# Optimization experiments

Hardware: AMD Instinct MI355X
Metric: run time of the kernel (lower is better)

Reference implementation:

```python
import jax, jax.numpy as jnp
import numpy as np

B, S, D, H = 16, 2048, 128, 4
HD = D // H  # 32
EPS = 1e-5


def layer_norm(x, g, b):
    m = jnp.mean(x, axis=-1, keepdims=True)
    v = jnp.mean((x - m) ** 2, axis=-1, keepdims=True)
    return (x - m) * jax.lax.rsqrt(v + EPS) * g + b


def setup_inputs() -> dict:
    key = jax.random.key(0)
    ks = jax.random.split(key, 9)
    lin = lambda k: jax.random.normal(k, (D, D), dtype=jnp.float32) * 0.01  # [in, out]
    return {
        "input0": jax.random.normal(ks[0], (B, S, D), dtype=jnp.float32),
        "Wq": lin(ks[1]), "bq": jnp.zeros((D,), jnp.float32),
        "Wk": lin(ks[2]), "bk": jnp.zeros((D,), jnp.float32),
        "Wv": lin(ks[3]), "bv": jnp.zeros((D,), jnp.float32),
        "Wo": lin(ks[4]), "bo": jnp.zeros((D,), jnp.float32),
        "g1": jnp.ones((D,), jnp.float32), "b1": jnp.zeros((D,), jnp.float32),
        "W1": lin(ks[5]), "bf1": jnp.zeros((D,), jnp.float32),
        "W2": lin(ks[6]), "bf2": jnp.zeros((D,), jnp.float32),
        "g2": jnp.ones((D,), jnp.float32), "b2": jnp.zeros((D,), jnp.float32),
    }


def reference(input0, Wq, bq, Wk, bk, Wv, bv, Wo, bo, g1, b1, W1, bf1, W2, bf2, g2, b2):
    x = input0
    # multi-head attention (self-attention), dropout in eval mode (identity)
    q = (x @ Wq + bq).reshape(B, S, H, HD)
    k = (x @ Wk + bk).reshape(B, S, H, HD)
    v = (x @ Wv + bv).reshape(B, S, H, HD)
    scores = jnp.einsum("bqhd,bkhd->bhqk", q, k) / jnp.sqrt(jnp.float32(HD))
    weights = jax.nn.softmax(scores, axis=-1)
    attn = jnp.einsum("bhqk,bkhd->bqhd", weights, v).reshape(B, S, D)
    attn = attn @ Wo + bo
    attended = layer_norm(attn + x, g1, b1)
    # feed-forward; note residual uses x (not attended), faithful to source
    ff = jax.nn.relu(attended @ W1 + bf1) @ W2 + bf2
    return layer_norm(ff + x, g2, b2)
```

## Files before the change

kernel.cpp:

```cpp
#include <hip/hip_runtime.h>
#include <math.h>

#define NB   16
#define NS   2048
#define ND   128
#define NH   4
#define NHD  32
#define NROWS (NB * NS)

typedef unsigned short u16;
typedef __bf16 bf16x8 __attribute__((ext_vector_type(8)));
typedef float  f32x4  __attribute__((ext_vector_type(4)));
typedef float  f32x16 __attribute__((ext_vector_type(16)));

static __device__ __forceinline__ u16 f2bf(float a) {
    union { __bf16 h; u16 u; } t; t.h = (__bf16)a; return t.u;
}
static __device__ __forceinline__ unsigned int pk2(float a, float b) {
    union { __bf16 h[2]; unsigned int u; } t;
    t.h[0] = (__bf16)a; t.h[1] = (__bf16)b; return t.u;
}

#if __has_builtin(__builtin_amdgcn_exp2f)
#define EXP2(x) __builtin_amdgcn_exp2f(x)
#else
extern "C" __device__ float __ocml_native_exp2_f32(float);
#define EXP2(x) __ocml_native_exp2_f32(x)
#endif

#define QSCALE (0.17677669529663687f * 1.4426950408889634f)

__global__ __launch_bounds__(256) void prep_kernel(
    const float* __restrict__ x,
    const float* __restrict__ Wq, const float* __restrict__ Wk,
    const float* __restrict__ Wv, const float* __restrict__ Wo,
    const float* __restrict__ W1, const float* __restrict__ W2,
    u16* __restrict__ xb, u16* __restrict__ wt)
{
    const int blk = blockIdx.x, tid = threadIdx.x;
    if (blk < 2048) {
        size_t e0 = (size_t)blk * 2048 + (size_t)tid * 8;
        const float4* p = reinterpret_cast<const float4*>(x + e0);
        float4 f0 = p[0], f1 = p[1];
        int4 o;
        o.x = pk2(f0.x, f0.y); o.y = pk2(f0.z, f0.w);
        o.z = pk2(f1.x, f1.y); o.w = pk2(f1.z, f1.w);
        *reinterpret_cast<int4*>(xb + e0) = o;
    } else {
        const int wb   = blk - 2048;
        const int widx = wb >> 3, sub = wb & 7;
        const float* W = widx == 0 ? Wq : widx == 1 ? Wk : widx == 2 ? Wv
                       : widx == 3 ? Wo : widx == 4 ? W1 : W2;
        const int flat8 = sub * 256 + tid;
        const int n = flat8 >> 4, k0 = (flat8 & 15) * 8;
        float v[8];
        #pragma unroll
        for (int j = 0; j < 8; ++j) v[j] = W[(size_t)(k0 + j) * ND + n];
        int4 o;
        o.x = pk2(v[0], v[1]); o.y = pk2(v[2], v[3]);
        o.z = pk2(v[4], v[5]); o.w = pk2(v[6], v[7]);
        *reinterpret_cast<int4*>(wt + (size_t)widx * 16384 + (size_t)n * ND + k0) = o;
    }
}

__global__ __launch_bounds__(256) void qkv_mfma_kernel(
    const u16* __restrict__ xb,
    const u16* __restrict__ wtq, const u16* __restrict__ wtk, const u16* __restrict__ wtv,
    const float* __restrict__ bq, const float* __restrict__ bk, const float* __restrict__ bv,
    u16* __restrict__ qo, u16* __restrict__ kfo, u16* __restrict__ vfo)
{
    const int tid = threadIdx.x, lane = tid & 63, w = tid >> 6;
    const int n = lane & 15, c = lane >> 4;
    const int row0 = blockIdx.x * 64;
    const int grow = row0 + w * 16;

    bf16x8 a[4];
    #pragma unroll
    for (int kk = 0; kk < 4; ++kk)
        a[kk] = *reinterpret_cast<const bf16x8*>(xb + (size_t)(grow + n) * ND + kk * 32 + c * 8);

    f32x4 accq[8], acck[8], accv[8];
    #pragma unroll
    for (int nb = 0; nb < 8; ++nb) {
        accq[nb] = f32x4{0.f, 0.f, 0.f, 0.f};
        acck[nb] = f32x4{0.f, 0.f, 0.f, 0.f};
        accv[nb] = f32x4{0.f, 0.f, 0.f, 0.f};
    }

    #pragma unroll
    for (int kk = 0; kk < 4; ++kk) {
        #pragma unroll
        for (int nb = 0; nb < 8; ++nb) {
            const size_t boff = (size_t)(nb * 16 + n) * ND + kk * 32 + c * 8;
            bf16x8 bqf = *reinterpret_cast<const bf16x8*>(wtq + boff);
            bf16x8 bkf = *reinterpret_cast<const bf16x8*>(wtk + boff);
            bf16x8 bvf = *reinterpret_cast<const bf16x8*>(wtv + boff);
            accq[nb] = __builtin_amdgcn_mfma_f32_16x16x32_bf16(a[kk], bqf, accq[nb], 0, 0, 0);
            acck[nb] = __builtin_amdgcn_mfma_f32_16x16x32_bf16(a[kk], bkf, acck[nb], 0, 0, 0);
            accv[nb] = __builtin_amdgcn_mfma_f32_16x16x32_bf16(a[kk], bvf, accv[nb], 0, 0, 0);
        }
    }

    const int b   = row0 >> 11;
    const int sp0 = (row0 & (NS - 1)) + w * 16;

    #pragma unroll
    for (int nb = 0; nb < 8; ++nb) {
        const int col = nb * 16 + n, hh = col >> 5, d32 = col & 31;
        const float bqv = bq[col], bkv = bk[col], bvv = bv[col];
        const size_t kvb = ((size_t)b * NH + hh) * (NS * NHD);

        #pragma unroll
        for (int r = 0; r < 4; ++r)
            qo[kvb + (size_t)(sp0 + 4 * c + r) * NHD + d32] =
                f2bf((accq[nb][r] + bqv) * QSCALE);

        const int s = d32 >> 4, c2 = (d32 >> 3) & 1, j = d32 & 7;
        #pragma unroll
        for (int r = 0; r < 4; ++r) {
            const int key = sp0 + 4 * c + r;
            const int T = key >> 5, l5 = key & 31;
            kfo[kvb + (size_t)(T * 2 + s) * 512 + (size_t)(l5 + 32 * c2) * 8 + j] =
                f2bf(acck[nb][r] + bkv);
        }

        const int lanep = d32 + 32 * (c & 1);
        const int j0    = 4 * (c >> 1);
        float v0 = accv[nb][0] + bvv, v1 = accv[nb][1] + bvv;
        float v2 = accv[nb][2] + bvv, v3 = accv[nb][3] + bvv;
        *reinterpret_cast<uint2*>(
            vfo + kvb + (size_t)(sp0 >> 4) * 512 + (size_t)lanep * 8 + j0) =
            make_uint2(pk2(v0, v1), pk2(v2, v3));
    }
}

__global__ __launch_bounds__(256) void attn_mfma_kernel(
    const u16* __restrict__ qg,
    const u16* __restrict__ kfg,
    const u16* __restrict__ vfg,
    u16* __restrict__ ao)
{
    const int tid = threadIdx.x, lane = tid & 63, w = tid >> 6;
    const int bh = blockIdx.y, b = bh >> 2, h = bh & 3;
    const int n = lane & 31, hf = lane >> 5;
    const size_t fbase = (size_t)bh * (NS * NHD);
    const int q0w = blockIdx.x * 128 + w * 32;

    const bf16x8 qf0 = *reinterpret_cast<const bf16x8*>(
        qg + fbase + (size_t)(q0w + n) * NHD + 8 * hf);
    const bf16x8 qf1 = *reinterpret_cast<const bf16x8*>(
        qg + fbase + (size_t)(q0w + n) * NHD + 16 + 8 * hf);

    f32x16 ot, zz;
    #pragma unroll
    for (int i = 0; i < 16; ++i) { ot[i] = 0.f; zz[i] = 0.f; }
    float lp0 = 0.f, lp1 = 0.f, lp2 = 0.f, lp3 = 0.f;

    const u16* kf = kfg + fbase + (size_t)lane * 8;
    const u16* vf = vfg + fbase + (size_t)lane * 8;

    for (int t = 0; t < NS / 64; ++t) {
        const bf16x8 ka00 = *reinterpret_cast<const bf16x8*>(kf + (size_t)(4 * t + 0) * 512);
        const bf16x8 ka01 = *reinterpret_cast<const bf16x8*>(kf + (size_t)(4 * t + 1) * 512);
        const bf16x8 ka10 = *reinterpret_cast<const bf16x8*>(kf + (size_t)(4 * t + 2) * 512);
        const bf16x8 ka11 = *reinterpret_cast<const bf16x8*>(kf + (size_t)(4 * t + 3) * 512);
        const bf16x8 va0  = *reinterpret_cast<const bf16x8*>(vf + (size_t)(4 * t + 0) * 512);
        const bf16x8 va1  = *reinterpret_cast<const bf16x8*>(vf + (size_t)(4 * t + 1) * 512);
        const bf16x8 va2  = *reinterpret_cast<const bf16x8*>(vf + (size_t)(4 * t + 2) * 512);
        const bf16x8 va3  = *reinterpret_cast<const bf16x8*>(vf + (size_t)(4 * t + 3) * 512);

        f32x16 s0 = __builtin_amdgcn_mfma_f32_32x32x16_bf16(ka00, qf0, zz, 0, 0, 0);
        s0 = __builtin_amdgcn_mfma_f32_32x32x16_bf16(ka01, qf1, s0, 0, 0, 0);
        f32x16 s1 = __builtin_amdgcn_mfma_f32_32x32x16_bf16(ka10, qf0, zz, 0, 0, 0);
        s1 = __builtin_amdgcn_mfma_f32_32x32x16_bf16(ka11, qf1, s1, 0, 0, 0);

        {
            float p[16];
            #pragma unroll
            for (int r = 0; r < 16; ++r) p[r] = EXP2(s0[r]);
            lp0 += p[0] + p[4] + p[8]  + p[12];
            lp1 += p[1] + p[5] + p[9]  + p[13];
            lp2 += p[2] + p[6] + p[10] + p[14];
            lp3 += p[3] + p[7] + p[11] + p[15];
            union { unsigned int u[4]; bf16x8 v; } pw0, pw1;
            #pragma unroll
            for (int i = 0; i < 4; ++i) pw0.u[i] = pk2(p[2 * i], p[2 * i + 1]);
            #pragma unroll
            for (int i = 0; i < 4; ++i) pw1.u[i] = pk2(p[8 + 2 * i], p[9 + 2 * i]);
            ot = __builtin_amdgcn_mfma_f32_32x32x16_bf16(va0, pw0.v, ot, 0, 0, 0);
            ot = __builtin_amdgcn_mfma_f32_32x32x16_bf16(va1, pw1.v, ot, 0, 0, 0);
        }
        {
            float p[16];
            #pragma unroll
            for (int r = 0; r < 16; ++r) p[r] = EXP2(s1[r]);
            lp0 += p[0] + p[4] + p[8]  + p[12];
            lp1 += p[1] + p[5] + p[9]  + p[13];
            lp2 += p[2] + p[6] + p[10] + p[14];
            lp3 += p[3] + p[7] + p[11] + p[15];
            union { unsigned int u[4]; bf16x8 v; } pw0, pw1;
            #pragma unroll
            for (int i = 0; i < 4; ++i) pw0.u[i] = pk2(p[2 * i], p[2 * i + 1]);
            #pragma unroll
            for (int i = 0; i < 4; ++i) pw1.u[i] = pk2(p[8 + 2 * i], p[9 + 2 * i]);
            ot = __builtin_amdgcn_mfma_f32_32x32x16_bf16(va2, pw0.v, ot, 0, 0, 0);
            ot = __builtin_amdgcn_mfma_f32_32x32x16_bf16(va3, pw1.v, ot, 0, 0, 0);
        }
    }

    float lp = (lp0 + lp1) + (lp2 + lp3);
    const float dn  = lp + __shfl_xor(lp, 32);
    const float inv = 1.0f / dn;

    u16* orow = ao + ((size_t)b * NS + q0w + n) * ND + h * NHD + 4 * hf;
    #pragma unroll
    for (int g = 0; g < 4; ++g) {
        uint2 wv = make_uint2(pk2(ot[4 * g] * inv, ot[4 * g + 1] * inv),
                              pk2(ot[4 * g + 2] * inv, ot[4 * g + 3] * inv));
        *reinterpret_cast<uint2*>(orow + 8 * g) = wv;
    }
}

template <int MODE>
__global__ __launch_bounds__(256) void proj_kernel(
    const u16* __restrict__ A, const u16* __restrict__ Wt,
    const float* __restrict__ bias, const float* __restrict__ res,
    const float* __restrict__ gamma, const float* __restrict__ beta,
    u16* __restrict__ outb, float* __restrict__ outf)
{
    const int tid = threadIdx.x, lane = tid & 63, w = tid >> 6;
    const int n = lane & 15, c = lane >> 4;
    const int grow = blockIdx.x * 64 + w * 16;

    bf16x8 a[4];
    #pragma unroll
    for (int kk = 0; kk < 4; ++kk)
        a[kk] = *reinterpret_cast<const bf16x8*>(A + (size_t)(grow + n) * ND + kk * 32 + c * 8);

    f32x4 acc[8];
    #pragma unroll
    for (int nb = 0; nb < 8; ++nb) acc[nb] = f32x4{0.f, 0.f, 0.f, 0.f};

    #pragma unroll
    for (int kk = 0; kk < 4; ++kk) {
        #pragma unroll
        for (int nb = 0; nb < 8; ++nb) {
            bf16x8 bw = *reinterpret_cast<const bf16x8*>(
                Wt + (size_t)(nb * 16 + n) * ND + kk * 32 + c * 8);
            acc[nb] = __builtin_amdgcn_mfma_f32_16x16x32_bf16(a[kk], bw, acc[nb], 0, 0, 0);
        }
    }

    if (MODE == 2) {
        #pragma unroll
        for (int nb = 0; nb < 8; ++nb) {
            const int col = nb * 16 + n;
            const float bb = bias[col];
            #pragma unroll
            for (int r = 0; r < 4; ++r) {
                float vv = fmaxf(acc[nb][r] + bb, 0.f);
                outb[(size_t)(grow + 4 * c + r) * ND + col] = f2bf(vv);
            }
        }
    } else {
        float vals[8][4];
        float sr[4]  = {0.f, 0.f, 0.f, 0.f};
        float sr2[4] = {0.f, 0.f, 0.f, 0.f};
        #pragma unroll
        for (int nb = 0; nb < 8; ++nb) {
            const int col = nb * 16 + n;
            const float bb = bias[col];
            #pragma unroll
            for (int r = 0; r < 4; ++r) {
                float vv = acc[nb][r] + bb + res[(size_t)(grow + 4 * c + r) * ND + col];
                vals[nb][r] = vv;
                sr[r]  += vv;
                sr2[r] += vv * vv;
            }
        }
        #pragma unroll
        for (int m = 1; m < 16; m <<= 1) {
            #pragma unroll
            for (int r = 0; r < 4; ++r) {
                sr[r]  += __shfl_xor(sr[r],  m);
                sr2[r] += __shfl_xor(sr2[r], m);
            }
        }
        float mean[4], rstd[4];
        #pragma unroll
        for (int r = 0; r < 4; ++r) {
            mean[r] = sr[r] * (1.f / 128.f);
            float var = fmaf(-mean[r], mean[r], sr2[r] * (1.f / 128.f));
            rstd[r] = rsqrtf(var + 1e-5f);
        }
        #pragma unroll
        for (int nb = 0; nb < 8; ++nb) {
            const int col = nb * 16 + n;
            const float g = gamma[col], bt = beta[col];
            #pragma unroll
            for (int r = 0; r < 4; ++r) {
                float y = fmaf((vals[nb][r] - mean[r]) * rstd[r], g, bt);
                if (MODE == 1)
                    outb[(size_t)(grow + 4 * c + r) * ND + col] = f2bf(y);
                else
                    outf[(size_t)(grow + 4 * c + r) * ND + col] = y;
            }
        }
    }
}

extern "C" void kernel_launch(void* const* d_in, const int* in_sizes, int n_in,
                              void* d_out, int out_size, void* d_ws, size_t ws_size,
                              hipStream_t stream)
{
    const float* x   = (const float*)d_in[0];
    const float* Wq  = (const float*)d_in[1];
    const float* bq  = (const float*)d_in[2];
    const float* Wk  = (const float*)d_in[3];
    const float* bk  = (const float*)d_in[4];
    const float* Wv  = (const float*)d_in[5];
    const float* bv  = (const float*)d_in[6];
    const float* Wo  = (const float*)d_in[7];
    const float* bo  = (const float*)d_in[8];
    const float* g1  = (const float*)d_in[9];
    const float* b1  = (const float*)d_in[10];
    const float* W1  = (const float*)d_in[11];
    const float* bf1 = (const float*)d_in[12];
    const float* W2  = (const float*)d_in[13];
    const float* bf2 = (const float*)d_in[14];
    const float* g2  = (const float*)d_in[15];
    const float* b2  = (const float*)d_in[16];
    float* outp = (float*)d_out;

    const size_t NE = (size_t)NROWS * ND;
    u16* xb  = (u16*)d_ws;
    u16* wt  = xb + NE;
    u16* qb  = wt + 6 * 16384;
    u16* kfb = qb + NE;
    u16* vfb = kfb + NE;
    u16* aob = (u16*)d_out;
    u16* attended = xb;
    u16* hff      = qb;

    dim3 blk(256);
    prep_kernel<<<dim3(2048 + 48), blk, 0, stream>>>(x, Wq, Wk, Wv, Wo, W1, W2, xb, wt);
    qkv_mfma_kernel<<<dim3(NROWS / 64), blk, 0, stream>>>(
        xb, wt + 0 * 16384, wt + 1 * 16384, wt + 2 * 16384, bq, bk, bv, qb, kfb, vfb);
    attn_mfma_kernel<<<dim3(NS / 128, NB * NH), blk, 0, stream>>>(qb, kfb, vfb, aob);
    proj_kernel<1><<<dim3(NROWS / 64), blk, 0, stream>>>(
        aob, wt + 3 * 16384, bo, x, g1, b1, attended, nullptr);
    proj_kernel<2><<<dim3(NROWS / 64), blk, 0, stream>>>(
        attended, wt + 4 * 16384, bf1, nullptr, nullptr, nullptr, hff, nullptr);
    proj_kernel<3><<<dim3(NROWS / 64), blk, 0, stream>>>(
        hff, wt + 5 * 16384, bf2, x, g2, b2, nullptr, outp);
}
```

Before: 140.0 us.

## Fuse x conversion into QKV, split attention keys across waves, fuse tail projections

The separate x-to-bf16 conversion pass is dropped; the QKV kernel now reads fp32 x and packs to bf16 in registers. The attention kernel splits each query tile's key range across two waves, each wave taking half the keys, and merges the partial outputs and denominators through shared memory. This doubles the grid and shortens each wave's serial loop. The three projection kernels (Wo plus LN1, W1 plus ReLU, W2 plus LN2) become one tail kernel that keeps intermediates in an LDS tile, removing two global round trips and two launches. The cost is extra LDS traffic, barriers, and idle waves during the merge.

```diff
diff --git a/kernel.cpp b/kernel.cpp
--- a/kernel.cpp
+++ b/kernel.cpp
@@ -31,40 +31,28 @@
 #define QSCALE (0.17677669529663687f * 1.4426950408889634f)
 
 __global__ __launch_bounds__(256) void prep_kernel(
-    const float* __restrict__ x,
     const float* __restrict__ Wq, const float* __restrict__ Wk,
     const float* __restrict__ Wv, const float* __restrict__ Wo,
     const float* __restrict__ W1, const float* __restrict__ W2,
-    u16* __restrict__ xb, u16* __restrict__ wt)
+    u16* __restrict__ wt)
 {
-    const int blk = blockIdx.x, tid = threadIdx.x;
-    if (blk < 2048) {
-        size_t e0 = (size_t)blk * 2048 + (size_t)tid * 8;
-        const float4* p = reinterpret_cast<const float4*>(x + e0);
-        float4 f0 = p[0], f1 = p[1];
-        int4 o;
-        o.x = pk2(f0.x, f0.y); o.y = pk2(f0.z, f0.w);
-        o.z = pk2(f1.x, f1.y); o.w = pk2(f1.z, f1.w);
-        *reinterpret_cast<int4*>(xb + e0) = o;
-    } else {
-        const int wb   = blk - 2048;
-        const int widx = wb >> 3, sub = wb & 7;
-        const float* W = widx == 0 ? Wq : widx == 1 ? Wk : widx == 2 ? Wv
-                       : widx == 3 ? Wo : widx == 4 ? W1 : W2;
-        const int flat8 = sub * 256 + tid;
-        const int n = flat8 >> 4, k0 = (flat8 & 15) * 8;
-        float v[8];
-        #pragma unroll
-        for (int j = 0; j < 8; ++j) v[j] = W[(size_t)(k0 + j) * ND + n];
-        int4 o;
-        o.x = pk2(v[0], v[1]); o.y = pk2(v[2], v[3]);
-        o.z = pk2(v[4], v[5]); o.w = pk2(v[6], v[7]);
-        *reinterpret_cast<int4*>(wt + (size_t)widx * 16384 + (size_t)n * ND + k0) = o;
-    }
+    const int wb = blockIdx.x, tid = threadIdx.x;
+    const int widx = wb >> 3, sub = wb & 7;
+    const float* W = widx == 0 ? Wq : widx == 1 ? Wk : widx == 2 ? Wv
+                   : widx == 3 ? Wo : widx == 4 ? W1 : W2;
+    const int flat8 = sub * 256 + tid;
+    const int n = flat8 >> 4, k0 = (flat8 & 15) * 8;
+    float v[8];
+    #pragma unroll
+    for (int j = 0; j < 8; ++j) v[j] = W[(size_t)(k0 + j) * ND + n];
+    int4 o;
+    o.x = pk2(v[0], v[1]); o.y = pk2(v[2], v[3]);
+    o.z = pk2(v[4], v[5]); o.w = pk2(v[6], v[7]);
+    *reinterpret_cast<int4*>(wt + (size_t)widx * 16384 + (size_t)n * ND + k0) = o;
 }
 
 __global__ __launch_bounds__(256) void qkv_mfma_kernel(
-    const u16* __restrict__ xb,
+    const float* __restrict__ x,
     const u16* __restrict__ wtq, const u16* __restrict__ wtk, const u16* __restrict__ wtv,
     const float* __restrict__ bq, const float* __restrict__ bk, const float* __restrict__ bv,
     u16* __restrict__ qo, u16* __restrict__ kfo, u16* __restrict__ vfo)
@@ -76,8 +64,15 @@
 
     bf16x8 a[4];
     #pragma unroll
-    for (int kk = 0; kk < 4; ++kk)
-        a[kk] = *reinterpret_cast<const bf16x8*>(xb + (size_t)(grow + n) * ND + kk * 32 + c * 8);
+    for (int kk = 0; kk < 4; ++kk) {
+        const float* xp = x + (size_t)(grow + n) * ND + kk * 32 + c * 8;
+        float4 f0 = *reinterpret_cast<const float4*>(xp);
+        float4 f1 = *reinterpret_cast<const float4*>(xp + 4);
+        union { unsigned int u[4]; bf16x8 v; } t;
+        t.u[0] = pk2(f0.x, f0.y); t.u[1] = pk2(f0.z, f0.w);
+        t.u[2] = pk2(f1.x, f1.y); t.u[3] = pk2(f1.z, f1.w);
+        a[kk] = t.v;
+    }
 
     f32x4 accq[8], acck[8], accv[8];
     #pragma unroll
@@ -140,11 +135,15 @@
     const u16* __restrict__ vfg,
     u16* __restrict__ ao)
 {
+    __shared__ float Ol[2][64][17];
+    __shared__ float Dl[2][64];
+
     const int tid = threadIdx.x, lane = tid & 63, w = tid >> 6;
+    const int qhalf = w >> 1, khalf = w & 1;
     const int bh = blockIdx.y, b = bh >> 2, h = bh & 3;
     const int n = lane & 31, hf = lane >> 5;
     const size_t fbase = (size_t)bh * (NS * NHD);
-    const int q0w = blockIdx.x * 128 + w * 32;
+    const int q0w = blockIdx.x * 64 + qhalf * 32;
 
     const bf16x8 qf0 = *reinterpret_cast<const bf16x8*>(
         qg + fbase + (size_t)(q0w + n) * NHD + 8 * hf);
@@ -154,12 +153,12 @@
     f32x16 ot, zz;
     #pragma unroll
     for (int i = 0; i < 16; ++i) { ot[i] = 0.f; zz[i] = 0.f; }
-    float lp0 = 0.f, lp1 = 0.f, lp2 = 0.f, lp3 = 0.f;
-
-    const u16* kf = kfg + fbase + (size_t)lane * 8;
-    const u16* vf = vfg + fbase + (size_t)lane * 8;
-
-    for (int t = 0; t < NS / 64; ++t) {
+    float lp = 0.f;
+
+    const u16* kf = kfg + fbase + (size_t)lane * 8 + (size_t)khalf * (16 * 4) * 512;
+    const u16* vf = vfg + fbase + (size_t)lane * 8 + (size_t)khalf * (16 * 4) * 512;
+
+    for (int t = 0; t < 16; ++t) {
         const bf16x8 ka00 = *reinterpret_cast<const bf16x8*>(kf + (size_t)(4 * t + 0) * 512);
         const bf16x8 ka01 = *reinterpret_cast<const bf16x8*>(kf + (size_t)(4 * t + 1) * 512);
         const bf16x8 ka10 = *reinterpret_cast<const bf16x8*>(kf + (size_t)(4 * t + 2) * 512);
@@ -178,10 +177,11 @@
             float p[16];
             #pragma unroll
             for (int r = 0; r < 16; ++r) p[r] = EXP2(s0[r]);
-            lp0 += p[0] + p[4] + p[8]  + p[12];
-            lp1 += p[1] + p[5] + p[9]  + p[13];
-            lp2 += p[2] + p[6] + p[10] + p[14];
-            lp3 += p[3] + p[7] + p[11] + p[15];
+            float t0 = (p[0] + p[1]) + (p[2] + p[3]);
+            float t1 = (p[4] + p[5]) + (p[6] + p[7]);
+            float t2 = (p[8] + p[9]) + (p[10] + p[11]);
+            float t3 = (p[12] + p[13]) + (p[14] + p[15]);
+            lp += (t0 + t1) + (t2 + t3);
             union { unsigned int u[4]; bf16x8 v; } pw0, pw1;
             #pragma unroll
             for (int i = 0; i < 4; ++i) pw0.u[i] = pk2(p[2 * i], p[2 * i + 1]);
@@ -194,10 +194,11 @@
             float p[16];
             #pragma unroll
             for (int r = 0; r < 16; ++r) p[r] = EXP2(s1[r]);
-            lp0 += p[0] + p[4] + p[8]  + p[12];
-            lp1 += p[1] + p[5] + p[9]  + p[13];
-            lp2 += p[2] + p[6] + p[10] + p[14];
-            lp3 += p[3] + p[7] + p[11] + p[15];
+            float t0 = (p[0] + p[1]) + (p[2] + p[3]);
+            float t1 = (p[4] + p[5]) + (p[6] + p[7]);
+            float t2 = (p[8] + p[9]) + (p[10] + p[11]);
+            float t3 = (p[12] + p[13]) + (p[14] + p[15]);
+            lp += (t0 + t1) + (t2 + t3);
             union { unsigned int u[4]; bf16x8 v; } pw0, pw1;
             #pragma unroll
             for (int i = 0; i < 4; ++i) pw0.u[i] = pk2(p[2 * i], p[2 * i + 1]);
@@ -208,102 +209,174 @@
         }
     }
 
-    float lp = (lp0 + lp1) + (lp2 + lp3);
-    const float dn  = lp + __shfl_xor(lp, 32);
-    const float inv = 1.0f / dn;
-
-    u16* orow = ao + ((size_t)b * NS + q0w + n) * ND + h * NHD + 4 * hf;
-    #pragma unroll
-    for (int g = 0; g < 4; ++g) {
-        uint2 wv = make_uint2(pk2(ot[4 * g] * inv, ot[4 * g + 1] * inv),
-                              pk2(ot[4 * g + 2] * inv, ot[4 * g + 3] * inv));
-        *reinterpret_cast<uint2*>(orow + 8 * g) = wv;
-    }
-}
-
-template <int MODE>
-__global__ __launch_bounds__(256) void proj_kernel(
-    const u16* __restrict__ A, const u16* __restrict__ Wt,
-    const float* __restrict__ bias, const float* __restrict__ res,
-    const float* __restrict__ gamma, const float* __restrict__ beta,
-    u16* __restrict__ outb, float* __restrict__ outf)
+    float lpt = lp + __shfl_xor(lp, 32);
+
+    if (khalf) {
+        #pragma unroll
+        for (int i = 0; i < 16; ++i) Ol[qhalf][lane][i] = ot[i];
+        Dl[qhalf][lane] = lpt;
+    }
+    __syncthreads();
+    if (!khalf) {
+        #pragma unroll
+        for (int i = 0; i < 16; ++i) ot[i] += Ol[qhalf][lane][i];
+        const float dn  = lpt + Dl[qhalf][lane];
+        const float inv = 1.0f / dn;
+
+        u16* orow = ao + ((size_t)b * NS + q0w + n) * ND + h * NHD + 4 * hf;
+        #pragma unroll
+        for (int g = 0; g < 4; ++g) {
+            uint2 wv = make_uint2(pk2(ot[4 * g] * inv, ot[4 * g + 1] * inv),
+                                  pk2(ot[4 * g + 2] * inv, ot[4 * g + 3] * inv));
+            *reinterpret_cast<uint2*>(orow + 8 * g) = wv;
+        }
+    }
+}
+
+__global__ __launch_bounds__(256) void tail_kernel(
+    const u16* __restrict__ A0, const u16* __restrict__ wto,
+    const u16* __restrict__ wt1, const u16* __restrict__ wt2,
+    const float* __restrict__ bo, const float* __restrict__ bf1,
+    const float* __restrict__ bf2, const float* __restrict__ x,
+    const float* __restrict__ g1, const float* __restrict__ b1,
+    const float* __restrict__ g2, const float* __restrict__ b2,
+    float* __restrict__ outp)
 {
+    __shared__ __align__(16) u16 tile[64][136];
     const int tid = threadIdx.x, lane = tid & 63, w = tid >> 6;
     const int n = lane & 15, c = lane >> 4;
-    const int grow = blockIdx.x * 64 + w * 16;
+    const int row0 = blockIdx.x * 64;
+    const int grow = row0 + w * 16;
+    const int lrow = w * 16;
 
     bf16x8 a[4];
-    #pragma unroll
-    for (int kk = 0; kk < 4; ++kk)
-        a[kk] = *reinterpret_cast<const bf16x8*>(A + (size_t)(grow + n) * ND + kk * 32 + c * 8);
-
     f32x4 acc[8];
+
+    #pragma unroll
+    for (int kk = 0; kk < 4; ++kk)
+        a[kk] = *reinterpret_cast<const bf16x8*>(
+            A0 + (size_t)(grow + n) * ND + kk * 32 + c * 8);
     #pragma unroll
     for (int nb = 0; nb < 8; ++nb) acc[nb] = f32x4{0.f, 0.f, 0.f, 0.f};
-
-    #pragma unroll
-    for (int kk = 0; kk < 4; ++kk) {
+    #pragma unroll
+    for (int kk = 0; kk < 4; ++kk)
         #pragma unroll
         for (int nb = 0; nb < 8; ++nb) {
             bf16x8 bw = *reinterpret_cast<const bf16x8*>(
-                Wt + (size_t)(nb * 16 + n) * ND + kk * 32 + c * 8);
+                wto + (size_t)(nb * 16 + n) * ND + kk * 32 + c * 8);
             acc[nb] = __builtin_amdgcn_mfma_f32_16x16x32_bf16(a[kk], bw, acc[nb], 0, 0, 0);
         }
-    }
-
-    if (MODE == 2) {
-        #pragma unroll
-        for (int nb = 0; nb < 8; ++nb) {
-            const int col = nb * 16 + n;
-            const float bb = bias[col];
-            #pragma unroll
-            for (int r = 0; r < 4; ++r) {
-                float vv = fmaxf(acc[nb][r] + bb, 0.f);
-                outb[(size_t)(grow + 4 * c + r) * ND + col] = f2bf(vv);
-            }
-        }
-    } else {
+
+    {
         float vals[8][4];
         float sr[4]  = {0.f, 0.f, 0.f, 0.f};
         float sr2[4] = {0.f, 0.f, 0.f, 0.f};
         #pragma unroll
         for (int nb = 0; nb < 8; ++nb) {
             const int col = nb * 16 + n;
-            const float bb = bias[col];
+            const float bb = bo[col];
             #pragma unroll
             for (int r = 0; r < 4; ++r) {
-                float vv = acc[nb][r] + bb + res[(size_t)(grow + 4 * c + r) * ND + col];
+                float vv = acc[nb][r] + bb +
+                           x[(size_t)(grow + 4 * c + r) * ND + col];
                 vals[nb][r] = vv;
                 sr[r]  += vv;
                 sr2[r] += vv * vv;
             }
         }
         #pragma unroll
-        for (int m = 1; m < 16; m <<= 1) {
+        for (int m = 1; m < 16; m <<= 1)
             #pragma unroll
             for (int r = 0; r < 4; ++r) {
                 sr[r]  += __shfl_xor(sr[r],  m);
                 sr2[r] += __shfl_xor(sr2[r], m);
             }
-        }
-        float mean[4], rstd[4];
         #pragma unroll
         for (int r = 0; r < 4; ++r) {
-            mean[r] = sr[r] * (1.f / 128.f);
-            float var = fmaf(-mean[r], mean[r], sr2[r] * (1.f / 128.f));
-            rstd[r] = rsqrtf(var + 1e-5f);
-        }
+            float mean = sr[r] * (1.f / 128.f);
+            float var  = fmaf(-mean, mean, sr2[r] * (1.f / 128.f));
+            float rstd = rsqrtf(var + 1e-5f);
+            #pragma unroll
+            for (int nb = 0; nb < 8; ++nb) {
+                const int col = nb * 16 + n;
+                float y = fmaf((vals[nb][r] - mean) * rstd, g1[col], b1[col]);
+                tile[lrow + 4 * c + r][col] = f2bf(y);
+            }
+        }
+    }
+    __syncthreads();
+
+    #pragma unroll
+    for (int kk = 0; kk < 4; ++kk)
+        a[kk] = *reinterpret_cast<const bf16x8*>(&tile[lrow + n][kk * 32 + c * 8]);
+    __syncthreads();
+    #pragma unroll
+    for (int nb = 0; nb < 8; ++nb) acc[nb] = f32x4{0.f, 0.f, 0.f, 0.f};
+    #pragma unroll
+    for (int kk = 0; kk < 4; ++kk)
+        #pragma unroll
+        for (int nb = 0; nb < 8; ++nb) {
+            bf16x8 bw = *reinterpret_cast<const bf16x8*>(
+                wt1 + (size_t)(nb * 16 + n) * ND + kk * 32 + c * 8);
+            acc[nb] = __builtin_amdgcn_mfma_f32_16x16x32_bf16(a[kk], bw, acc[nb], 0, 0, 0);
+        }
+    #pragma unroll
+    for (int nb = 0; nb < 8; ++nb) {
+        const int col = nb * 16 + n;
+        const float bb = bf1[col];
+        #pragma unroll
+        for (int r = 0; r < 4; ++r)
+            tile[lrow + 4 * c + r][col] = f2bf(fmaxf(acc[nb][r] + bb, 0.f));
+    }
+    __syncthreads();
+
+    #pragma unroll
+    for (int kk = 0; kk < 4; ++kk)
+        a[kk] = *reinterpret_cast<const bf16x8*>(&tile[lrow + n][kk * 32 + c * 8]);
+    #pragma unroll
+    for (int nb = 0; nb < 8; ++nb) acc[nb] = f32x4{0.f, 0.f, 0.f, 0.f};
+    #pragma unroll
+    for (int kk = 0; kk < 4; ++kk)
+        #pragma unroll
+        for (int nb = 0; nb < 8; ++nb) {
+            bf16x8 bw = *reinterpret_cast<const bf16x8*>(
+                wt2 + (size_t)(nb * 16 + n) * ND + kk * 32 + c * 8);
+            acc[nb] = __builtin_amdgcn_mfma_f32_16x16x32_bf16(a[kk], bw, acc[nb], 0, 0, 0);
+        }
+    {
+        float vals[8][4];
+        float sr[4]  = {0.f, 0.f, 0.f, 0.f};
+        float sr2[4] = {0.f, 0.f, 0.f, 0.f};
         #pragma unroll
         for (int nb = 0; nb < 8; ++nb) {
             const int col = nb * 16 + n;
-            const float g = gamma[col], bt = beta[col];
+            const float bb = bf2[col];
             #pragma unroll
             for (int r = 0; r < 4; ++r) {
-                float y = fmaf((vals[nb][r] - mean[r]) * rstd[r], g, bt);
-                if (MODE == 1)
-                    outb[(size_t)(grow + 4 * c + r) * ND + col] = f2bf(y);
-                else
-                    outf[(size_t)(grow + 4 * c + r) * ND + col] = y;
+                float vv = acc[nb][r] + bb +
+                           x[(size_t)(grow + 4 * c + r) * ND + col];
+                vals[nb][r] = vv;
+                sr[r]  += vv;
+                sr2[r] += vv * vv;
+            }
+        }
+        #pragma unroll
+        for (int m = 1; m < 16; m <<= 1)
+            #pragma unroll
+            for (int r = 0; r < 4; ++r) {
+                sr[r]  += __shfl_xor(sr[r],  m);
+                sr2[r] += __shfl_xor(sr2[r], m);
+            }
+        #pragma unroll
+        for (int r = 0; r < 4; ++r) {
+            float mean = sr[r] * (1.f / 128.f);
+            float var  = fmaf(-mean, mean, sr2[r] * (1.f / 128.f));
+            float rstd = rsqrtf(var + 1e-5f);
+            #pragma unroll
+            for (int nb = 0; nb < 8; ++nb) {
+                const int col = nb * 16 + n;
+                float y = fmaf((vals[nb][r] - mean) * rstd, g2[col], b2[col]);
+                outp[(size_t)(grow + 4 * c + r) * ND + col] = y;
             }
         }
     }
@@ -333,24 +406,18 @@
     float* outp = (float*)d_out;
 
     const size_t NE = (size_t)NROWS * ND;
-    u16* xb  = (u16*)d_ws;
-    u16* wt  = xb + NE;
+    u16* wt  = (u16*)d_ws;
     u16* qb  = wt + 6 * 16384;
     u16* kfb = qb + NE;
     u16* vfb = kfb + NE;
-    u16* aob = (u16*)d_out;
-    u16* attended = xb;
-    u16* hff      = qb;
+    u16* aob = vfb + NE;
 
     dim3 blk(256);
-    prep_kernel<<<dim3(2048 + 48), blk, 0, stream>>>(x, Wq, Wk, Wv, Wo, W1, W2, xb, wt);
+    prep_kernel<<<dim3(48), blk, 0, stream>>>(Wq, Wk, Wv, Wo, W1, W2, wt);
     qkv_mfma_kernel<<<dim3(NROWS / 64), blk, 0, stream>>>(
-        xb, wt + 0 * 16384, wt + 1 * 16384, wt + 2 * 16384, bq, bk, bv, qb, kfb, vfb);
-    attn_mfma_kernel<<<dim3(NS / 128, NB * NH), blk, 0, stream>>>(qb, kfb, vfb, aob);
-    proj_kernel<1><<<dim3(NROWS / 64), blk, 0, stream>>>(
-        aob, wt + 3 * 16384, bo, x, g1, b1, attended, nullptr);
-    proj_kernel<2><<<dim3(NROWS / 64), blk, 0, stream>>>(
-        attended, wt + 4 * 16384, bf1, nullptr, nullptr, nullptr, hff, nullptr);
-    proj_kernel<3><<<dim3(NROWS / 64), blk, 0, stream>>>(
-        hff, wt + 5 * 16384, bf2, x, g2, b2, nullptr, outp);
-}
+        x, wt + 0 * 16384, wt + 1 * 16384, wt + 2 * 16384, bq, bk, bv, qb, kfb, vfb);
+    attn_mfma_kernel<<<dim3(NS / 64, NB * NH), blk, 0, stream>>>(qb, kfb, vfb, aob);
+    tail_kernel<<<dim3(NROWS / 64), blk, 0, stream>>>(
+        aob, wt + 3 * 16384, wt + 4 * 16384, wt + 5 * 16384,
+        bo, bf1, bf2, x, g1, b1, g2, b2, outp);
+}
```

New measurement: 129.6 us. 7.4% less time.
